# Kernel tuning notes

Hardware: AMD Instinct MI355X
Metric: run time of the kernel (lower is better)

## Reference

```python
import jax, jax.numpy as jnp
import numpy as np

B, S, D, MAXDUR = 16, 4096, 256, 8


def setup_inputs() -> dict:
    key = jax.random.key(0)
    k1, k2 = jax.random.split(key)
    x = jax.random.normal(k1, (B, S, D), dtype=jnp.float32)
    # per-timestep repeat counts (durations); original takes float and rounds,
    # int values make round/cast an identity
    dimensions = jax.random.randint(k2, (B, S, 1), 0, MAXDUR).astype(jnp.int32)
    return {"x": x, "dimensions": dimensions}


def reference(x, dimensions):
    # Faithful math of the TF Expand layer, expressed as a single gather with
    # cumulative offsets instead of tile(seq_len*max_dim)+mask+RaggedTensor.
    d = jnp.round(jnp.squeeze(dimensions, -1).astype(jnp.float32)).astype(jnp.int32)  # [B,S]
    totals = jnp.sum(d, axis=1)                       # [B] expanded length per example
    T = int(np.asarray(jnp.max(totals)))              # padded output length (batch max)
    csum = jnp.cumsum(d, axis=1)                      # [B,S] row boundaries
    pos = jnp.arange(T)                               # [T]
    # source index for each output frame: first s with csum[s] > pos
    idx = jax.vmap(lambda c: jnp.searchsorted(c, pos, side='right'))(csum)  # [B,T]
    idx = jnp.minimum(idx, d.shape[1] - 1)            # clamp padding region
    out = jnp.take_along_axis(x, idx[:, :, None], axis=1)  # [B,T,D] gather
    mask = (pos[None, :] < totals[:, None]).astype(x.dtype)  # zero-pad like to_tensor()
    return out * mask[:, :, None]
```

## Files before the change

kernel.cpp:

```cpp
#include <hip/hip_runtime.h>

#define BATCH 16
#define SEQ   4096
#define DIM   256

#define SCATTER_BLOCKS (BATCH * SEQ / 4)
#define TAILC 128

typedef float f32x4 __attribute__((ext_vector_type(4)));

__global__ __launch_bounds__(1024) void scan_kernel(const int* __restrict__ dims,
                                                    int* __restrict__ csum,
                                                    int* __restrict__ totals) {
    __shared__ int wsum[16];
    const int b    = blockIdx.x;
    const int tid  = threadIdx.x;
    const int lane = tid & 63;
    const int wave = tid >> 6;

    const int4 dv = ((const int4*)(dims + b * SEQ))[tid];
    const int p0 = dv.x;
    const int p1 = p0 + dv.y;
    const int p2 = p1 + dv.z;
    const int p3 = p2 + dv.w;
    int v = p3;

    #pragma unroll
    for (int off = 1; off < 64; off <<= 1) {
        int n = __shfl_up(v, off, 64);
        if (lane >= off) v += n;
    }
    if (lane == 63) wsum[wave] = v;
    __syncthreads();

    if (tid == 0) {
        int run = 0;
        #pragma unroll
        for (int i = 0; i < 16; ++i) { int t = wsum[i]; wsum[i] = run; run += t; }
        totals[b] = run;
    }
    __syncthreads();

    const int excl = wsum[wave] + (v - p3);
    int4 o;
    o.x = excl + p0; o.y = excl + p1; o.z = excl + p2; o.w = excl + p3;
    ((int4*)(csum + b * SEQ))[tid] = o;
}

__global__ __launch_bounds__(256) void expand_kernel(const float* __restrict__ x,
                                                     const int* __restrict__ csum,
                                                     const int* __restrict__ totals,
                                                     float* __restrict__ out,
                                                     int T) {
    const int lane = threadIdx.x & 63;
    const int wave = threadIdx.x >> 6;

    if (blockIdx.x < SCATTER_BLOCKS) {
        const int wv  = blockIdx.x * 4 + wave;
        const int b   = wv >> 12;
        const int s   = wv & (SEQ - 1);

        int start, end;
        if (s != 0) {
            const int2 se = *(const int2*)(csum + wv - 1);
            start = se.x; end = se.y;
        } else {
            start = 0;   end = csum[wv];
        }
        const int cnt = end - start;
        if (cnt <= 0) return;

        const f32x4 row = __builtin_nontemporal_load(
            ((const f32x4*)x) + (size_t)wv * (DIM / 4) + lane);
        f32x4* dst = (f32x4*)out + ((size_t)b * T + start) * (DIM / 4) + lane;

        #pragma unroll
        for (int j = 0; j < 7; ++j) {
            if (j < cnt) dst[j * (DIM / 4)] = row;
        }
        for (int j = 7; j < cnt; ++j)
            dst[j * (DIM / 4)] = row;
    } else {
        const int idx   = blockIdx.x - SCATTER_BLOCKS;
        const int b     = idx / TAILC;
        const int chunk = idx % TAILC;
        const int t0    = totals[b];
        const f32x4 z   = {0.f, 0.f, 0.f, 0.f};
        for (int t = t0 + chunk * 4 + wave; t < T; t += 2 * TAILC * 4) {
            ((f32x4*)out)[((size_t)b * T + t) * (DIM / 4) + lane] = z;
            const int t2 = t + TAILC * 4;
            if (t2 < T)
                ((f32x4*)out)[((size_t)b * T + t2) * (DIM / 4) + lane] = z;
        }
    }
}

extern "C" void kernel_launch(void* const* d_in, const int* in_sizes, int n_in,
                              void* d_out, int out_size, void* d_ws, size_t ws_size,
                              hipStream_t stream) {
    const float* x    = (const float*)d_in[0];
    const int*   dims = (const int*)d_in[1];
    float*       out  = (float*)d_out;

    const int T = out_size / (BATCH * DIM);

    int* totals = (int*)d_ws;
    int* csum   = totals + 64;

    scan_kernel<<<BATCH, 1024, 0, stream>>>(dims, csum, totals);
    expand_kernel<<<SCATTER_BLOCKS + BATCH * TAILC, 256, 0, stream>>>(
        x, csum, totals, out, T);
}
```

Measured before the change: 280.6 us.

## Replace scatter-expand with index map built in scan plus gather kernel

```diff
diff --git a/kernel.cpp b/kernel.cpp
--- a/kernel.cpp
+++ b/kernel.cpp
@@ -4,15 +4,15 @@
 #define SEQ   4096
 #define DIM   256
 
-#define SCATTER_BLOCKS (BATCH * SEQ / 4)
-#define TAILC 128
-
 typedef float f32x4 __attribute__((ext_vector_type(4)));
 
 __global__ __launch_bounds__(1024) void scan_kernel(const int* __restrict__ dims,
                                                     int* __restrict__ csum,
-                                                    int* __restrict__ totals) {
+                                                    int* __restrict__ totals,
+                                                    int* __restrict__ idx,
+                                                    int T) {
     __shared__ int wsum[16];
+    __shared__ int stot;
     const int b    = blockIdx.x;
     const int tid  = threadIdx.x;
     const int lane = tid & 63;
@@ -38,14 +38,54 @@
         #pragma unroll
         for (int i = 0; i < 16; ++i) { int t = wsum[i]; wsum[i] = run; run += t; }
         totals[b] = run;
+        stot      = run;
     }
     __syncthreads();
 
     const int excl = wsum[wave] + (v - p3);
-    int4 o;
-    o.x = excl + p0; o.y = excl + p1; o.z = excl + p2; o.w = excl + p3;
-    ((int4*)(csum + b * SEQ))[tid] = o;
+
+    if (idx) {
+        int* __restrict__ ib = idx + (size_t)b * T;
+        const int s0 = tid * 4;
+        const int st0 = excl,      en0 = excl + p0;
+        const int st1 = en0,       en1 = excl + p1;
+        const int st2 = en1,       en2 = excl + p2;
+        const int st3 = en2,       en3 = excl + p3;
+        for (int k = st0; k < en0; ++k) ib[k] = s0;
+        for (int k = st1; k < en1; ++k) ib[k] = s0 + 1;
+        for (int k = st2; k < en2; ++k) ib[k] = s0 + 2;
+        for (int k = st3; k < en3; ++k) ib[k] = s0 + 3;
+        for (int t = stot + tid; t < T; t += 1024) ib[t] = -1;
+    } else {
+        int4 o;
+        o.x = excl + p0; o.y = excl + p1; o.z = excl + p2; o.w = excl + p3;
+        ((int4*)(csum + b * SEQ))[tid] = o;
+    }
 }
+
+__global__ __launch_bounds__(256) void gather_kernel(const float* __restrict__ x,
+                                                     const int* __restrict__ idx,
+                                                     float* __restrict__ out,
+                                                     int T) {
+    const int lane = threadIdx.x & 63;
+    const int wave = threadIdx.x >> 6;
+    const int b    = blockIdx.y;
+    const int t    = blockIdx.x * 4 + wave;
+    if (t >= T) return;
+
+    const int s = idx[(size_t)b * T + t];
+    f32x4* dst = (f32x4*)out + ((size_t)b * T + t) * (DIM / 4) + lane;
+    if (s < 0) {
+        const f32x4 z = {0.f, 0.f, 0.f, 0.f};
+        *dst = z;
+        return;
+    }
+    const f32x4 row = ((const f32x4*)x)[((size_t)b * SEQ + s) * (DIM / 4) + lane];
+    *dst = row;
+}
+
+#define SCATTER_BLOCKS (BATCH * SEQ / 4)
+#define TAILC 128
 
 __global__ __launch_bounds__(256) void expand_kernel(const float* __restrict__ x,
                                                      const int* __restrict__ csum,
@@ -102,12 +142,25 @@
     const int*   dims = (const int*)d_in[1];
     float*       out  = (float*)d_out;
 
-    const int T = out_size / (BATCH * DIM);
+    const int T = out_size / (BATCH * DIM * (int)sizeof(float)) > 0
+                    ? out_size / (BATCH * DIM * (int)sizeof(float))
+                    : out_size / (BATCH * DIM);
+    const int Tf = out_size / (BATCH * DIM);
 
     int* totals = (int*)d_ws;
     int* csum   = totals + 64;
+    int* idxmap = csum + BATCH * SEQ;
 
-    scan_kernel<<<BATCH, 1024, 0, stream>>>(dims, csum, totals);
-    expand_kernel<<<SCATTER_BLOCKS + BATCH * TAILC, 256, 0, stream>>>(
-        x, csum, totals, out, T);
+    const size_t need = (size_t)(64 + BATCH * SEQ) * 4 + (size_t)BATCH * Tf * 4;
+
+    if (ws_size >= need) {
+        scan_kernel<<<BATCH, 1024, 0, stream>>>(dims, csum, totals, idxmap, Tf);
+        dim3 grid((Tf + 3) / 4, BATCH);
+        gather_kernel<<<grid, 256, 0, stream>>>(x, idxmap, out, Tf);
+    } else {
+        scan_kernel<<<BATCH, 1024, 0, stream>>>(dims, csum, totals, nullptr, Tf);
+        expand_kernel<<<SCATTER_BLOCKS + BATCH * TAILC, 256, 0, stream>>>(
+            x, csum, totals, out, Tf);
+    }
+    (void)T;
 }
```

Result: slower. 302.2 us (+7.7%).

## Switch expand to output-partitioned persistent waves with binary search and row prefetch

Applied to the files above, without the earlier changes.

```diff
diff --git a/kernel.cpp b/kernel.cpp
--- a/kernel.cpp
+++ b/kernel.cpp
@@ -4,8 +4,8 @@
 #define SEQ   4096
 #define DIM   256
 
-#define SCATTER_BLOCKS (BATCH * SEQ / 4)
-#define TAILC 128
+#define GPB   512
+#define EXP_BLOCKS (BATCH * GPB / 4)
 
 typedef float f32x4 __attribute__((ext_vector_type(4)));
 
@@ -47,52 +47,60 @@
     ((int4*)(csum + b * SEQ))[tid] = o;
 }
 
-__global__ __launch_bounds__(256) void expand_kernel(const float* __restrict__ x,
-                                                     const int* __restrict__ csum,
-                                                     const int* __restrict__ totals,
-                                                     float* __restrict__ out,
-                                                     int T) {
+__global__ __launch_bounds__(256) void expand_persist(const float* __restrict__ x,
+                                                      const int* __restrict__ csum,
+                                                      const int* __restrict__ totals,
+                                                      float* __restrict__ out,
+                                                      int T) {
     const int lane = threadIdx.x & 63;
-    const int wave = threadIdx.x >> 6;
+    const int gw   = blockIdx.x * 4 + (threadIdx.x >> 6);
+    const int b    = gw >> 9;
+    const int q    = gw & (GPB - 1);
+    const int span = (T + GPB - 1) / GPB;
 
-    if (blockIdx.x < SCATTER_BLOCKS) {
-        const int wv  = blockIdx.x * 4 + wave;
-        const int b   = wv >> 12;
-        const int s   = wv & (SEQ - 1);
+    int t = q * span;
+    const int tend = min(t + span, T);
+    if (t >= tend) return;
 
-        int start, end;
-        if (s != 0) {
-            const int2 se = *(const int2*)(csum + wv - 1);
-            start = se.x; end = se.y;
-        } else {
-            start = 0;   end = csum[wv];
+    const int total = totals[b];
+    const int* __restrict__ cs   = csum + b * SEQ;
+    const f32x4* __restrict__ xb = (const f32x4*)x + (size_t)b * SEQ * (DIM / 4);
+    f32x4* __restrict__ ob       = (f32x4*)out + (size_t)b * T * (DIM / 4) + lane;
+
+    if (t < total) {
+        int lo = 0, hi = SEQ;
+        while (lo < hi) {
+            const int mid = (lo + hi) >> 1;
+            if (cs[mid] <= t) lo = mid + 1; else hi = mid;
         }
-        const int cnt = end - start;
-        if (cnt <= 0) return;
+        int   s_cur = lo;
+        int   e_cur = cs[s_cur];
+        f32x4 r_cur = __builtin_nontemporal_load(xb + (size_t)s_cur * (DIM / 4) + lane);
 
-        const f32x4 row = __builtin_nontemporal_load(
-            ((const f32x4*)x) + (size_t)wv * (DIM / 4) + lane);
-        f32x4* dst = (f32x4*)out + ((size_t)b * T + start) * (DIM / 4) + lane;
+        while (true) {
+            int s_nxt = s_cur + 1;
+            int e_nxt = e_cur;
+            while (s_nxt < SEQ) {
+                const int c = cs[s_nxt];
+                if (c > e_cur) { e_nxt = c; break; }
+                ++s_nxt;
+            }
+            const bool have = (s_nxt < SEQ);
+            f32x4 r_nxt;
+            if (have)
+                r_nxt = __builtin_nontemporal_load(xb + (size_t)s_nxt * (DIM / 4) + lane);
 
-        #pragma unroll
-        for (int j = 0; j < 7; ++j) {
-            if (j < cnt) dst[j * (DIM / 4)] = row;
-        }
-        for (int j = 7; j < cnt; ++j)
-            dst[j * (DIM / 4)] = row;
-    } else {
-        const int idx   = blockIdx.x - SCATTER_BLOCKS;
-        const int b     = idx / TAILC;
-        const int chunk = idx % TAILC;
-        const int t0    = totals[b];
-        const f32x4 z   = {0.f, 0.f, 0.f, 0.f};
-        for (int t = t0 + chunk * 4 + wave; t < T; t += 2 * TAILC * 4) {
-            ((f32x4*)out)[((size_t)b * T + t) * (DIM / 4) + lane] = z;
-            const int t2 = t + TAILC * 4;
-            if (t2 < T)
-                ((f32x4*)out)[((size_t)b * T + t2) * (DIM / 4) + lane] = z;
+            const int lim = min(e_cur, tend);
+            for (; t < lim; ++t) ob[(size_t)t * (DIM / 4)] = r_cur;
+
+            if (t >= tend) return;
+            if (!have) break;
+            s_cur = s_nxt; e_cur = e_nxt; r_cur = r_nxt;
         }
     }
+
+    const f32x4 z = {0.f, 0.f, 0.f, 0.f};
+    for (; t < tend; ++t) ob[(size_t)t * (DIM / 4)] = z;
 }
 
 extern "C" void kernel_launch(void* const* d_in, const int* in_sizes, int n_in,
@@ -108,6 +116,5 @@
     int* csum   = totals + 64;
 
     scan_kernel<<<BATCH, 1024, 0, stream>>>(dims, csum, totals);
-    expand_kernel<<<SCATTER_BLOCKS + BATCH * TAILC, 256, 0, stream>>>(
-        x, csum, totals, out, T);
+    expand_persist<<<EXP_BLOCKS, 256, 0, stream>>>(x, csum, totals, out, T);
 }
```

Result: slower. 305.4 us (+8.8%).
